# Kernel optimization log

Hardware: AMD Instinct MI355X
Metric: run time of the kernel (lower is better)

## Reference

```python
import jax, jax.numpy as jnp
import numpy as np

B, C, H, W = 4, 256, 96, 96
PARA, MOD, NH = 256, 256, 128
PI = 3.14159  # constant used in the torch source (not math.pi)


def setup_inputs():
    key = jax.random.key(0)
    ks = jax.random.split(key, 16)
    w = lambda k, shp: jax.random.normal(k, shp, jnp.float32) * 0.02
    z = lambda n: jnp.zeros((n,), jnp.float32)
    return {
        "feature_map": jax.random.normal(ks[0], (B, C, H, W), jnp.float32),
        "para_code": jax.random.normal(ks[1], (B, PARA), jnp.float32),
        "style_code": jax.random.normal(ks[2], (B, MOD), jnp.float32),
        "lin_common_w": w(ks[3], (PARA, PARA)), "lin_common_b": z(PARA),
        "lin_scale_w": w(ks[4], (PARA, C)), "lin_scale_b": z(C),
        "lin_rot_w": w(ks[5], (PARA, C)), "lin_rot_b": z(C),
        "lin_trans_w": w(ks[6], (PARA, 2 * C)), "lin_trans_b": z(2 * C),
        "a1_shared_w": w(ks[7], (MOD, NH)), "a1_shared_b": z(NH),
        "a1_gamma_w": w(ks[8], (NH, C)), "a1_gamma_b": z(C),
        "a1_beta_w": w(ks[9], (NH, C)), "a1_beta_b": z(C),
        "conv1_w": w(ks[10], (C, C, 3, 3)), "conv1_b": z(C),
        "a2_shared_w": w(ks[11], (MOD, NH)), "a2_shared_b": z(NH),
        "a2_gamma_w": w(ks[12], (NH, C)), "a2_gamma_b": z(C),
        "a2_beta_w": w(ks[13], (NH, C)), "a2_beta_b": z(C),
        "conv2_w": w(ks[14], (C, C, 3, 3)), "conv2_b": z(C),
    }


def _adaat(fm, pc, cw, cb, sw, sb, rw, rb, tw, tb):
    # fm: [B,C,H,W]; per-channel 2D affine warp, channels act as depth of a 3D grid_sample.
    Bn, Cn, Hn, Wn = fm.shape
    pc = jax.nn.relu(pc @ cw + cb)
    scale = jax.nn.sigmoid(pc @ sw + sb) * 2.0            # [B,C]
    angle = jnp.tanh(pc @ rw + rb) * PI                   # [B,C]
    trans = jnp.tanh(pc @ tw + tb).reshape(Bn, Cn, 2)     # [B,C,2]
    cos = jnp.cos(angle)[:, :, None, None]
    sin = jnp.sin(angle)[:, :, None, None]
    sc = scale[:, :, None, None]
    tx = trans[:, :, 0][:, :, None, None]
    ty = trans[:, :, 1][:, :, None, None]
    # align_corners=True style normalized source grid (as in make_coordinate_grid_3d)
    gx = (2.0 * jnp.arange(Wn) / (Wn - 1) - 1.0)[None, :]  # [1,W]
    gy = (2.0 * jnp.arange(Hn) / (Hn - 1) - 1.0)[:, None]  # [H,1]
    # rotation [[cos,-sin],[sin,cos]] @ [x,y], then scale + translate -> [B,C,H,W]
    xw = (cos * gx - sin * gy) * sc + tx
    yw = (sin * gx + cos * gy) * sc + ty
    gz = 2.0 * jnp.arange(Cn) / (Cn - 1) - 1.0             # [C]
    # unnormalize with align_corners=False (torch grid_sample default)
    ix = ((xw + 1.0) * Wn - 1.0) * 0.5
    iy = ((yw + 1.0) * Hn - 1.0) * 0.5
    iz = (((gz + 1.0) * Cn - 1.0) * 0.5)[None, :, None, None]  # [1,C,1,1]
    x0 = jnp.floor(ix); y0 = jnp.floor(iy); z0 = jnp.floor(iz)
    wx = ix - x0; wy = iy - y0; wz = iz - z0
    x0 = x0.astype(jnp.int32); y0 = y0.astype(jnp.int32); z0 = z0.astype(jnp.int32)
    bidx = jnp.arange(Bn)[:, None, None, None]

    def gather(zi, yi, xi):
        valid = (zi >= 0) & (zi < Cn) & (yi >= 0) & (yi < Hn) & (xi >= 0) & (xi < Wn)
        v = fm[bidx, jnp.clip(zi, 0, Cn - 1), jnp.clip(yi, 0, Hn - 1), jnp.clip(xi, 0, Wn - 1)]
        return jnp.where(valid, v, 0.0)

    out = jnp.zeros_like(fm)
    for dz, wzc in ((0, 1.0 - wz), (1, wz)):
        for dy, wyc in ((0, 1.0 - wy), (1, wy)):
            for dx, wxc in ((0, 1.0 - wx), (1, wx)):
                out = out + gather(z0 + dz, y0 + dy, x0 + dx) * (wzc * wyc * wxc)
    return out


def _adain_layer(x, style, shw, shb, gw, gb, bw, bb):
    m = x.mean(axis=(2, 3), keepdims=True)
    v = x.var(axis=(2, 3), keepdims=True)  # biased, as torch InstanceNorm2d
    xn = (x - m) / jnp.sqrt(v + 1e-5)
    a = jax.nn.relu(style @ shw + shb)
    gamma = (a @ gw + gb)[:, :, None, None]
    beta = (a @ bw + bb)[:, :, None, None]
    return xn * (1.0 + gamma) + beta


def _conv3(x, w, b):
    y = jax.lax.conv_general_dilated(x, w, (1, 1), ((1, 1), (1, 1)),
                                     dimension_numbers=("NCHW", "OIHW", "NCHW"))
    return y + b[None, :, None, None]


def _lrelu(x):
    return jnp.where(x >= 0, x, 0.2 * x)


def reference(feature_map, para_code, style_code,
              lin_common_w, lin_common_b, lin_scale_w, lin_scale_b,
              lin_rot_w, lin_rot_b, lin_trans_w, lin_trans_b,
              a1_shared_w, a1_shared_b, a1_gamma_w, a1_gamma_b, a1_beta_w, a1_beta_b,
              conv1_w, conv1_b,
              a2_shared_w, a2_shared_b, a2_gamma_w, a2_gamma_b, a2_beta_w, a2_beta_b,
              conv2_w, conv2_b):
    t = _adaat(feature_map, para_code, lin_common_w, lin_common_b,
               lin_scale_w, lin_scale_b, lin_rot_w, lin_rot_b, lin_trans_w, lin_trans_b)
    x = _adain_layer(t, style_code, a1_shared_w, a1_shared_b, a1_gamma_w, a1_gamma_b, a1_beta_w, a1_beta_b)
    x = _conv3(_lrelu(x), conv1_w, conv1_b)
    x = _adain_layer(x, style_code, a2_shared_w, a2_shared_b, a2_gamma_w, a2_gamma_b, a2_beta_w, a2_beta_b)
    x = _conv3(_lrelu(x), conv2_w, conv2_b)
    return x
```

## Files before the change

### kernel.cpp

```cpp
#include <hip/hip_runtime.h>
#include <hip/hip_bf16.h>
#include <cstddef>

#define BATCH 4
#define CH 256
#define HH 96
#define WW 96
#define HWN (HH*WW)
#define NTOT (BATCH*CH*HWN)
#define XT_H 98
#define XT_W 98
#define XT_PLANE (XT_H*XT_W*CH)

typedef __attribute__((ext_vector_type(16))) float f32x16;
typedef __attribute__((ext_vector_type(8))) __bf16 bfrag;
typedef __attribute__((ext_vector_type(8))) unsigned short u16x8;

static __device__ __forceinline__ unsigned short f2bf(float f) {
  unsigned int u = __float_as_uint(f);
  unsigned int r = (u + 0x7fffu + ((u >> 16) & 1u)) >> 16;
  return (unsigned short)r;
}

static __device__ __forceinline__ void gload16(const unsigned short* g,
                                               unsigned short* l) {
  __builtin_amdgcn_global_load_lds(
      (const __attribute__((address_space(1))) unsigned int*)g,
      (__attribute__((address_space(3))) unsigned int*)l, 16, 0, 0);
}

__global__ __launch_bounds__(256) void params_stage1_kernel(
    const float* __restrict__ para, const float* __restrict__ style,
    const float* __restrict__ cw,  const float* __restrict__ cb,
    const float* __restrict__ a1w, const float* __restrict__ a1b,
    const float* __restrict__ a2w, const float* __restrict__ a2b,
    float* __restrict__ pcbuf, float* __restrict__ a1buf, float* __restrict__ a2buf)
{
  __shared__ float s_in[256];
  __shared__ float red[256];
  int part = blockIdx.x, b = blockIdx.y, t = threadIdx.x;
  s_in[t] = (part < 4) ? para[b*256 + t] : style[b*256 + t];
  __syncthreads();
  if (part < 4) {
    int o = t & 63, ks = t >> 6, co0 = part * 64;
    const float* wcol = cw + co0 + o;
    float acc = 0.f;
    #pragma unroll 8
    for (int i = 0; i < 64; i++) {
      int k = ks * 64 + i;
      acc = fmaf(s_in[k], wcol[k * 256], acc);
    }
    red[t] = acc;
    __syncthreads();
    if (t < 64) {
      float s = red[t] + red[t + 64] + red[t + 128] + red[t + 192];
      pcbuf[b*256 + co0 + t] = fmaxf(s + cb[co0 + t], 0.f);
    }
  } else {
    const float* w  = (part == 4) ? a1w : a2w;
    const float* bb = (part == 4) ? a1b : a2b;
    float* outp = (part == 4) ? a1buf : a2buf;
    int o = t & 127, ks = t >> 7;
    const float* wcol = w + o;
    float acc = 0.f;
    #pragma unroll 8
    for (int i = 0; i < 128; i++) {
      int k = ks * 128 + i;
      acc = fmaf(s_in[k], wcol[k * 128], acc);
    }
    red[t] = acc;
    __syncthreads();
    if (t < 128) {
      float s = red[t] + red[t + 128];
      outp[b*128 + t] = fmaxf(s + bb[t], 0.f);
    }
  }
}

__global__ __launch_bounds__(256) void params_stage2_kernel(
    const float* __restrict__ pcbuf, const float* __restrict__ a1buf,
    const float* __restrict__ a2buf,
    const float* __restrict__ sw,  const float* __restrict__ sb,
    const float* __restrict__ rw,  const float* __restrict__ rb,
    const float* __restrict__ tw,  const float* __restrict__ tb,
    const float* __restrict__ g1w, const float* __restrict__ g1b,
    const float* __restrict__ b1w, const float* __restrict__ b1b,
    const float* __restrict__ g2w, const float* __restrict__ g2b,
    const float* __restrict__ b2w, const float* __restrict__ b2b,
    float* __restrict__ warp, float* __restrict__ gb1, float* __restrict__ gb2)
{
  __shared__ float s_pc[256], s_a1[128], s_a2[128];
  __shared__ float red[8][4][16];
  int co0 = blockIdx.x * 16, b = blockIdx.y, t = threadIdx.x;
  s_pc[t] = pcbuf[b*256 + t];
  if (t < 128) s_a1[t] = a1buf[b*128 + t];
  else         s_a2[t - 128] = a2buf[b*128 + (t - 128)];
  __syncthreads();

  int cl = t & 15, klane = t >> 4;
  int c = co0 + cl;
  const float2* tw2 = (const float2*)tw;
  float ds = 0.f, dr = 0.f, dtx = 0.f, dty = 0.f;
  float g1 = 0.f, be1 = 0.f, g2 = 0.f, be2 = 0.f;
  #pragma unroll 4
  for (int kk = 0; kk < 16; kk++) {
    int i = klane * 16 + kk;
    float p = s_pc[i];
    ds  = fmaf(p, sw[i*256 + c], ds);
    dr  = fmaf(p, rw[i*256 + c], dr);
    float2 tv = tw2[i*256 + c];
    dtx = fmaf(p, tv.x, dtx);
    dty = fmaf(p, tv.y, dty);
  }
  #pragma unroll 4
  for (int kk = 0; kk < 8; kk++) {
    int i = klane * 8 + kk;
    float a = s_a1[i];
    g1  = fmaf(a, g1w[i*256 + c], g1);
    be1 = fmaf(a, b1w[i*256 + c], be1);
    float a2v = s_a2[i];
    g2  = fmaf(a2v, g2w[i*256 + c], g2);
    be2 = fmaf(a2v, b2w[i*256 + c], be2);
  }
  ds  += __shfl_down(ds, 32, 64);  ds  += __shfl_down(ds, 16, 64);
  dr  += __shfl_down(dr, 32, 64);  dr  += __shfl_down(dr, 16, 64);
  dtx += __shfl_down(dtx, 32, 64); dtx += __shfl_down(dtx, 16, 64);
  dty += __shfl_down(dty, 32, 64); dty += __shfl_down(dty, 16, 64);
  g1  += __shfl_down(g1, 32, 64);  g1  += __shfl_down(g1, 16, 64);
  be1 += __shfl_down(be1, 32, 64); be1 += __shfl_down(be1, 16, 64);
  g2  += __shfl_down(g2, 32, 64);  g2  += __shfl_down(g2, 16, 64);
  be2 += __shfl_down(be2, 32, 64); be2 += __shfl_down(be2, 16, 64);
  int wv = t >> 6;
  if ((t & 63) < 16) {
    red[0][wv][cl] = ds;  red[1][wv][cl] = dr;
    red[2][wv][cl] = dtx; red[3][wv][cl] = dty;
    red[4][wv][cl] = g1;  red[5][wv][cl] = be1;
    red[6][wv][cl] = g2;  red[7][wv][cl] = be2;
  }
  __syncthreads();
  if (t < 16) {
    float v[8];
    #pragma unroll
    for (int o = 0; o < 8; o++)
      v[o] = red[o][0][t] + red[o][1][t] + red[o][2][t] + red[o][3][t];
    int cc = co0 + t;
    int bc = b*256 + cc;
    float scale = 2.f / (1.f + expf(-(v[0] + sb[cc])));
    float ang = tanhf(v[1] + rb[cc]) * 3.14159f;
    float sn, cs;
    sincosf(ang, &sn, &cs);
    warp[bc*4 + 0] = cs * scale;
    warp[bc*4 + 1] = sn * scale;
    warp[bc*4 + 2] = tanhf(v[2] + tb[2*cc]);
    warp[bc*4 + 3] = tanhf(v[3] + tb[2*cc + 1]);
    gb1[bc*2]     = v[4] + g1b[cc];
    gb1[bc*2 + 1] = v[5] + b1b[cc];
    gb2[bc*2]     = v[6] + g2b[cc];
    gb2[bc*2 + 1] = v[7] + b2b[cc];
  }
}

__global__ __launch_bounds__(256) void prep_weights_kernel(
    const float* __restrict__ w1, const float* __restrict__ w2,
    unsigned short* __restrict__ wf1, unsigned short* __restrict__ wf2)
{
  int co = blockIdx.x & 255;
  const float* src = (blockIdx.x < 256) ? w1 : w2;
  unsigned short* dst = (blockIdx.x < 256) ? wf1 : wf2;
  int ci = threadIdx.x;
  int coblk = co >> 6, m = (co >> 5) & 1;
  int l = (co & 31) | (((ci >> 3) & 1) << 5);
  int ks = ci >> 4, j = ci & 7;
  const float* p = src + ((size_t)co * 256 + ci) * 9;
  #pragma unroll
  for (int tap = 0; tap < 9; tap++) {
    size_t idx = (((size_t)((coblk * 16 + ks) * 9 + tap) * 2 + m) * 64 + l) * 8 + j;
    dst[idx] = f2bf(p[tap]);
  }
}

__global__ __launch_bounds__(256) void adaat_kernel(
    const float* __restrict__ fm, const float* __restrict__ warp,
    const float* __restrict__ gb1, float* __restrict__ tout,
    float* __restrict__ nrm1)
{
  __shared__ float s[96 * 100];
  int bc = blockIdx.x;
  int b = bc >> 8, c = bc & 255;
  float csc = warp[bc*4 + 0], ssc = warp[bc*4 + 1];
  float tx = warp[bc*4 + 2], ty = warp[bc*4 + 3];

  const float axw = csc * (96.f / 95.f);
  const float axh = -ssc * (96.f / 95.f);
  const float ax0 = 48.f * (tx - csc + ssc) + 47.5f;
  const float ayw = ssc * (96.f / 95.f);
  const float ayh = csc * (96.f / 95.f);
  const float ay0 = 48.f * (ty - ssc - csc) + 47.5f;

  float iz = 256.f * (float)c / 255.f - 0.5f;
  float z0f = floorf(iz);
  float wz = iz - z0f;
  int z0 = (int)z0f;
  const float* p0 = (z0 >= 0) ? fm + (size_t)(b*256 + z0) * HWN : nullptr;
  const float* p1 = (z0 + 1 < 256) ? fm + (size_t)(b*256 + z0 + 1) * HWN : nullptr;
  float w0 = 1.f - wz, w1 = wz;

  int t = threadIdx.x;
  const float4* q0 = (const float4*)p0;
  const float4* q1 = (const float4*)p1;
  for (int i = t; i < 2304; i += 256) {
    int row = i / 24, col = i - row * 24;
    float4 r = {0.f, 0.f, 0.f, 0.f};
    if (q0) {
      float4 v = q0[i];
      r.x = w0 * v.x; r.y = w0 * v.y; r.z = w0 * v.z; r.w = w0 * v.w;
    }
    if (q1) {
      float4 v = q1[i];
      r.x = fmaf(w1, v.x, r.x); r.y = fmaf(w1, v.y, r.y);
      r.z = fmaf(w1, v.z, r.z); r.w = fmaf(w1, v.w, r.w);
    }
    *(float4*)&s[row * 100 + col * 4] = r;
  }
  __syncthreads();

  int h = t / 96, w = t - (t / 96) * 96;
  float* dst = tout + (size_t)bc * HWN;
  float sum = 0.f, sumsq = 0.f;
  #pragma unroll
  for (int k = 0; k < 36; k++) {
    float ix = fmaf(axw, (float)w, fmaf(axh, (float)h, ax0));
    float iy = fmaf(ayw, (float)w, fmaf(ayh, (float)h, ay0));
    float x0f = floorf(ix), y0f = floorf(iy);
    float wx = ix - x0f, wy = iy - y0f;
    int x0 = (int)x0f, y0 = (int)y0f;
    int x0c = min(max(x0, 0), 95), x1c = min(max(x0 + 1, 0), 95);
    int y0c = min(max(y0, 0), 95), y1c = min(max(y0 + 1, 0), 95);
    bool vx0 = (unsigned)x0 < 96u, vx1 = (unsigned)(x0 + 1) < 96u;
    bool vy0 = (unsigned)y0 < 96u, vy1 = (unsigned)(y0 + 1) < 96u;
    float a00 = s[y0c * 100 + x0c], a01 = s[y0c * 100 + x1c];
    float a10 = s[y1c * 100 + x0c], a11 = s[y1c * 100 + x1c];
    float wxm = 1.f - wx, wym = 1.f - wy;
    float w00 = (vy0 && vx0) ? wym * wxm : 0.f;
    float w01 = (vy0 && vx1) ? wym * wx  : 0.f;
    float w10 = (vy1 && vx0) ? wy * wxm  : 0.f;
    float w11 = (vy1 && vx1) ? wy * wx   : 0.f;
    float v = w00 * a00;
    v = fmaf(w01, a01, v);
    v = fmaf(w10, a10, v);
    v = fmaf(w11, a11, v);
    dst[t + k * 256] = v;
    sum += v;
    sumsq = fmaf(v, v, sumsq);
    int wn = w + 64;
    int carry = (wn >= 96) ? 1 : 0;
    w = wn - (carry ? 96 : 0);
    h += 2 + carry;
  }

  for (int off = 32; off > 0; off >>= 1) {
    sum   += __shfl_down(sum, off, 64);
    sumsq += __shfl_down(sumsq, off, 64);
  }
  __shared__ float rs[4], rq[4];
  int lane = t & 63, wvi = t >> 6;
  if (lane == 0) { rs[wvi] = sum; rq[wvi] = sumsq; }
  __syncthreads();
  if (t == 0) {
    float S = rs[0] + rs[1] + rs[2] + rs[3];
    float Q = rq[0] + rq[1] + rq[2] + rq[3];
    float m = S * (1.f / 9216.f);
    float var = Q * (1.f / 9216.f) - m * m;
    float rstd = rsqrtf(var + 1e-5f);
    float sc = (1.f + gb1[bc*2]) * rstd;
    nrm1[bc*2] = sc;
    nrm1[bc*2 + 1] = gb1[bc*2 + 1] - m * sc;
  }
}

__global__ __launch_bounds__(256) void finalize_stats_kernel(
    const float* __restrict__ psum, const float* __restrict__ gb,
    float* __restrict__ nrm)
{
  int bc = blockIdx.x * 256 + threadIdx.x;
  int b = bc >> 8, co = bc & 255;
  float S = 0.f, Q = 0.f;
  for (int j = 0; j < 96; j++) {
    const float* p = psum + ((((size_t)b * 48 + (j >> 1)) * 2 + (j & 1)) * 256 + co) * 2;
    S += p[0];
    Q += p[1];
  }
  float m = S * (1.f / 9216.f);
  float var = Q * (1.f / 9216.f) - m * m;
  float rstd = rsqrtf(var + 1e-5f);
  float sc = (1.f + gb[bc*2]) * rstd;
  nrm[bc*2] = sc;
  nrm[bc*2 + 1] = gb[bc*2 + 1] - m * sc;
}

__global__ __launch_bounds__(256) void transpose_norm_kernel(
    const float* __restrict__ x, const float* __restrict__ nrm,
    unsigned short* __restrict__ xt)
{
  int hi = blockIdx.x;
  int b  = blockIdx.y;
  unsigned short* dst = xt + (size_t)b * XT_PLANE + (size_t)hi * (XT_W * CH);
  int t = threadIdx.x;
  int h = hi - 1;
  u16x8 zero = {0,0,0,0,0,0,0,0};
  if (h < 0 || h >= 96) {
    for (int c = t; c < XT_W * CH / 8; c += 256) ((u16x8*)dst)[c] = zero;
    return;
  }
  __shared__ unsigned short s[96 * 256];
  int ci = t;
  float sc = nrm[(b*256 + ci)*2], bi = nrm[(b*256 + ci)*2 + 1];
  const float* src = x + ((size_t)(b*256 + ci)) * HWN + h * 96;
  for (int wg = 0; wg < 24; wg++) {
    float4 v = *(const float4*)(src + wg * 4);
    float y0 = fmaf(v.x, sc, bi); y0 = (y0 >= 0.f) ? y0 : 0.2f * y0;
    float y1 = fmaf(v.y, sc, bi); y1 = (y1 >= 0.f) ? y1 : 0.2f * y1;
    float y2 = fmaf(v.z, sc, bi); y2 = (y2 >= 0.f) ? y2 : 0.2f * y2;
    float y3 = fmaf(v.w, sc, bi); y3 = (y3 >= 0.f) ? y3 : 0.2f * y3;
    s[(wg*4 + 0) * 256 + ci] = f2bf(y0);
    s[(wg*4 + 1) * 256 + ci] = f2bf(y1);
    s[(wg*4 + 2) * 256 + ci] = f2bf(y2);
    s[(wg*4 + 3) * 256 + ci] = f2bf(y3);
  }
  __syncthreads();
  for (int c = t; c < 98 * 32; c += 256) {
    int w = c >> 5, p = c & 31;
    u16x8 v = zero;
    if (w >= 1 && w <= 96) v = *(const u16x8*)&s[(w - 1) * 256 + p * 8];
    ((u16x8*)dst)[c] = v;
  }
}

__global__ __launch_bounds__(256, 3) void conv_mfma_kernel(
    const unsigned short* __restrict__ xt,
    const unsigned short* __restrict__ wf,
    const float* __restrict__ cb,
    float* __restrict__ out,
    float* __restrict__ psum)
{
  __shared__ __align__(16) unsigned short s_in[2][784 * 8];

  int hb = blockIdx.x, coblk = blockIdx.y, b = blockIdx.z;
  int co0 = coblk * 64, h0 = hb * 2;
  int t = threadIdx.x, lane = t & 63, wv = t >> 6;
  int rw = wv >> 1, mh = wv & 1;
  int l31 = lane & 31, lhi = lane >> 5;
  const unsigned short* xtb = xt + (size_t)b * XT_PLANE;

  int pre_g[4];
  #pragma unroll
  for (int i = 0; i < 4; i++) {
    int c = t + i * 256;
    if (c < 784) {
      int r = c / 196;
      int rem = c - r * 196;
      int half = rem / 98;
      int w = rem - half * 98;
      pre_g[i] = ((h0 + r) * 98 + w) * 256 + half * 8;
    }
  }

  f32x16 acc[3];
  #pragma unroll
  for (int n = 0; n < 3; n++)
    #pragma unroll
    for (int i = 0; i < 16; i++) acc[n][i] = 0.f;

  const unsigned short* wfb = wf + (size_t)(coblk * 16) * 9216 + mh * 512 + lane * 8;

  {
    #pragma unroll
    for (int i = 0; i < 3; i++)
      gload16(xtb + pre_g[i], &s_in[0][(i * 256 + wv * 64) * 8]);
    u16x8 tail;
    if (t < 16) tail = *(const u16x8*)(xtb + pre_g[3]);
    if (t < 16) *(u16x8*)(&s_in[0][(768 + t) * 8]) = tail;
  }
  bfrag wa[9];
  #pragma unroll
  for (int tap = 0; tap < 9; tap++) wa[tap] = *(const bfrag*)(wfb + tap * 1024);
  __syncthreads();

  int buf = 0;
  u16x8 tail;
  #pragma unroll 1
  for (int ks = 0; ks < 16; ks++) {
    if (ks < 15) {
      int cib = (ks + 1) * 16;
      unsigned short* nb = s_in[buf ^ 1];
      #pragma unroll
      for (int i = 0; i < 3; i++)
        gload16(xtb + pre_g[i] + cib, &nb[(i * 256 + wv * 64) * 8]);
      if (t < 16) tail = *(const u16x8*)(xtb + pre_g[3] + cib);
    }
    const unsigned short* sb = s_in[buf];
    int ksn = (ks < 15) ? (ks + 1) : 15;
    const unsigned short* wkn = wfb + (size_t)ksn * 9216;
    #pragma unroll
    for (int ky = 0; ky < 3; ky++) {
      const unsigned short* srow = sb + (((rw + ky) * 2 + lhi) * 98) * 8;
      bfrag bb[9];
      #pragma unroll
      for (int kx = 0; kx < 3; kx++)
        #pragma unroll
        for (int n = 0; n < 3; n++)
          bb[kx * 3 + n] = *(const bfrag*)(srow + (n * 32 + kx + l31) * 8);
      __builtin_amdgcn_s_setprio(1);
      #pragma unroll
      for (int kx = 0; kx < 3; kx++) {
        int tap = ky * 3 + kx;
        acc[0] = __builtin_amdgcn_mfma_f32_32x32x16_bf16(wa[tap], bb[kx*3+0], acc[0], 0, 0, 0);
        acc[1] = __builtin_amdgcn_mfma_f32_32x32x16_bf16(wa[tap], bb[kx*3+1], acc[1], 0, 0, 0);
        acc[2] = __builtin_amdgcn_mfma_f32_32x32x16_bf16(wa[tap], bb[kx*3+2], acc[2], 0, 0, 0);
        wa[tap] = *(const bfrag*)(wkn + tap * 1024);
      }
      __builtin_amdgcn_s_setprio(0);
    }
    if (ks < 15 && t < 16) *(u16x8*)(&s_in[buf ^ 1][(768 + t) * 8]) = tail;
    __syncthreads();
    buf ^= 1;
  }

  int h = h0 + rw;
  float bsum[16], bsq[16];
  #pragma unroll
  for (int r = 0; r < 16; r++) {
    int row = (r & 3) + 8 * (r >> 2) + 4 * lhi;
    int co = co0 + mh * 32 + row;
    float bv = cb[co];
    size_t base = ((size_t)(b * 256 + co) * 96 + h) * 96;
    float s = 0.f, q = 0.f;
    #pragma unroll
    for (int n = 0; n < 3; n++) {
      float y = acc[n][r] + bv;
      out[base + n * 32 + l31] = y;
      s += y;
      q = fmaf(y, y, q);
    }
    bsum[r] = s; bsq[r] = q;
  }
  if (psum) {
    #pragma unroll
    for (int r = 0; r < 16; r++) {
      float s = bsum[r], q = bsq[r];
      #pragma unroll
      for (int off = 16; off > 0; off >>= 1) {
        s += __shfl_xor(s, off, 64);
        q += __shfl_xor(q, off, 64);
      }
      bsum[r] = s; bsq[r] = q;
    }
    if (l31 == 0) {
      float* pp = psum + ((((size_t)b * 48 + hb) * 2 + rw) * 256) * 2;
      #pragma unroll
      for (int r = 0; r < 16; r++) {
        int row = (r & 3) + 8 * (r >> 2) + 4 * lhi;
        int co = co0 + mh * 32 + row;
        pp[co * 2]     = bsum[r];
        pp[co * 2 + 1] = bsq[r];
      }
    }
  }
}

extern "C" void kernel_launch(void* const* d_in, const int* in_sizes, int n_in,
                              void* d_out, int out_size, void* d_ws, size_t ws_size,
                              hipStream_t stream)
{
  const float* fm    = (const float*)d_in[0];
  const float* para  = (const float*)d_in[1];
  const float* style = (const float*)d_in[2];
  const float* cw  = (const float*)d_in[3];
  const float* cb  = (const float*)d_in[4];
  const float* sw  = (const float*)d_in[5];
  const float* sb  = (const float*)d_in[6];
  const float* rw  = (const float*)d_in[7];
  const float* rb  = (const float*)d_in[8];
  const float* tw  = (const float*)d_in[9];
  const float* tb  = (const float*)d_in[10];
  const float* a1w = (const float*)d_in[11];
  const float* a1b = (const float*)d_in[12];
  const float* g1w = (const float*)d_in[13];
  const float* g1b = (const float*)d_in[14];
  const float* b1w = (const float*)d_in[15];
  const float* b1b = (const float*)d_in[16];
  const float* c1w = (const float*)d_in[17];
  const float* c1b = (const float*)d_in[18];
  const float* a2w = (const float*)d_in[19];
  const float* a2b = (const float*)d_in[20];
  const float* g2w = (const float*)d_in[21];
  const float* g2b = (const float*)d_in[22];
  const float* b2w = (const float*)d_in[23];
  const float* b2b = (const float*)d_in[24];
  const float* c2w = (const float*)d_in[25];
  const float* c2b = (const float*)d_in[26];

  float* outf = (float*)d_out;

  unsigned short* xtbuf = (unsigned short*)d_ws;
  unsigned short* wf1   = xtbuf + (size_t)BATCH * XT_PLANE;
  unsigned short* wf2   = wf1 + 9 * 256 * 256;
  float* fws  = (float*)(wf2 + 9 * 256 * 256);
  float* warp = fws;
  float* gb1  = warp + 4 * 1024;
  float* gb2  = gb1 + 2 * 1024;
  float* nrm1 = gb2 + 2 * 1024;
  float* nrm2 = nrm1 + 2 * 1024;
  float* pcbuf = nrm2 + 2 * 1024;
  float* a1buf = pcbuf + 1024;
  float* a2buf = a1buf + 512;
  float* psum  = a2buf + 512;

  params_stage1_kernel<<<dim3(6, 4), 256, 0, stream>>>(para, style, cw, cb,
      a1w, a1b, a2w, a2b, pcbuf, a1buf, a2buf);
  params_stage2_kernel<<<dim3(16, 4), 256, 0, stream>>>(pcbuf, a1buf, a2buf,
      sw, sb, rw, rb, tw, tb, g1w, g1b, b1w, b1b, g2w, g2b, b2w, b2b,
      warp, gb1, gb2);
  prep_weights_kernel<<<512, 256, 0, stream>>>(c1w, c2w, wf1, wf2);
  adaat_kernel<<<1024, 256, 0, stream>>>(fm, warp, gb1, outf, nrm1);
  transpose_norm_kernel<<<dim3(98, 4), 256, 0, stream>>>(outf, nrm1, xtbuf);
  conv_mfma_kernel<<<dim3(48, 4, 4), 256, 0, stream>>>(xtbuf, wf1, c1b, outf, psum);
  finalize_stats_kernel<<<4, 256, 0, stream>>>(psum, gb2, nrm2);
  transpose_norm_kernel<<<dim3(98, 4), 256, 0, stream>>>(outf, nrm2, xtbuf);
  conv_mfma_kernel<<<dim3(48, 4, 4), 256, 0, stream>>>(xtbuf, wf2, c2b, outf, nullptr);
}
```

Measured before the change: 188.9 us.

## Give each conv wave both 32-channel output halves, halving block size

The conv kernel drops from 4 waves to 2 waves per block, and each wave now computes both 32-row output-channel halves (a 64x96 tile) instead of one. Each B fragment loaded from LDS is reused by two MFMAs, which halves LDS reads per MFMA and shrinks the block. The cost is double the accumulators and weight registers per thread (6 accumulators, 18 weight fragments), which pushes register pressure up. Launch bounds change to 128 threads with 2 blocks per SIMD hint, and each thread does twice as many staging loads.

```diff
diff --git a/kernel.cpp b/kernel.cpp
--- a/kernel.cpp
+++ b/kernel.cpp
@@ -336,7 +336,7 @@
   }
 }
 
-__global__ __launch_bounds__(256, 3) void conv_mfma_kernel(
+__global__ __launch_bounds__(128, 2) void conv_mfma_kernel(
     const unsigned short* __restrict__ xt,
     const unsigned short* __restrict__ wf,
     const float* __restrict__ cb,
@@ -348,62 +348,72 @@
   int hb = blockIdx.x, coblk = blockIdx.y, b = blockIdx.z;
   int co0 = coblk * 64, h0 = hb * 2;
   int t = threadIdx.x, lane = t & 63, wv = t >> 6;
-  int rw = wv >> 1, mh = wv & 1;
   int l31 = lane & 31, lhi = lane >> 5;
   const unsigned short* xtb = xt + (size_t)b * XT_PLANE;
 
-  int pre_g[4];
-  #pragma unroll
-  for (int i = 0; i < 4; i++) {
-    int c = t + i * 256;
-    if (c < 784) {
-      int r = c / 196;
-      int rem = c - r * 196;
-      int half = rem / 98;
-      int w = rem - half * 98;
-      pre_g[i] = ((h0 + r) * 98 + w) * 256 + half * 8;
-    }
-  }
-
-  f32x16 acc[3];
-  #pragma unroll
-  for (int n = 0; n < 3; n++)
+  int pre_g[6];
+  #pragma unroll
+  for (int i = 0; i < 6; i++) {
+    int c = t + i * 128;
+    int r = c / 196;
+    int rem = c - r * 196;
+    int half = rem / 98;
+    int w = rem - half * 98;
+    pre_g[i] = ((h0 + r) * 98 + w) * 256 + half * 8;
+  }
+  int tail_g = 0;
+  if (t < 16) {
+    int c = 768 + t;
+    int r = c / 196;
+    int rem = c - r * 196;
+    int half = rem / 98;
+    int w = rem - half * 98;
+    tail_g = ((h0 + r) * 98 + w) * 256 + half * 8;
+  }
+
+  f32x16 acc[2][3];
+  #pragma unroll
+  for (int m = 0; m < 2; m++)
     #pragma unroll
-    for (int i = 0; i < 16; i++) acc[n][i] = 0.f;
-
-  const unsigned short* wfb = wf + (size_t)(coblk * 16) * 9216 + mh * 512 + lane * 8;
-
-  {
-    #pragma unroll
-    for (int i = 0; i < 3; i++)
-      gload16(xtb + pre_g[i], &s_in[0][(i * 256 + wv * 64) * 8]);
-    u16x8 tail;
-    if (t < 16) tail = *(const u16x8*)(xtb + pre_g[3]);
-    if (t < 16) *(u16x8*)(&s_in[0][(768 + t) * 8]) = tail;
-  }
-  bfrag wa[9];
-  #pragma unroll
-  for (int tap = 0; tap < 9; tap++) wa[tap] = *(const bfrag*)(wfb + tap * 1024);
+    for (int n = 0; n < 3; n++)
+      #pragma unroll
+      for (int i = 0; i < 16; i++) acc[m][n][i] = 0.f;
+
+  const unsigned short* wfb = wf + (size_t)(coblk * 16) * 9216 + lane * 8;
+
+  #pragma unroll
+  for (int i = 0; i < 6; i++)
+    gload16(xtb + pre_g[i], &s_in[0][(i * 128 + wv * 64) * 8]);
+  u16x8 tl;
+  if (t < 16) {
+    tl = *(const u16x8*)(xtb + tail_g);
+    *(u16x8*)(&s_in[0][(768 + t) * 8]) = tl;
+  }
+  bfrag wa[9][2];
+  #pragma unroll
+  for (int tap = 0; tap < 9; tap++) {
+    wa[tap][0] = *(const bfrag*)(wfb + tap * 1024);
+    wa[tap][1] = *(const bfrag*)(wfb + tap * 1024 + 512);
+  }
   __syncthreads();
 
   int buf = 0;
-  u16x8 tail;
   #pragma unroll 1
   for (int ks = 0; ks < 16; ks++) {
     if (ks < 15) {
       int cib = (ks + 1) * 16;
       unsigned short* nb = s_in[buf ^ 1];
       #pragma unroll
-      for (int i = 0; i < 3; i++)
-        gload16(xtb + pre_g[i] + cib, &nb[(i * 256 + wv * 64) * 8]);
-      if (t < 16) tail = *(const u16x8*)(xtb + pre_g[3] + cib);
+      for (int i = 0; i < 6; i++)
+        gload16(xtb + pre_g[i] + cib, &nb[(i * 128 + wv * 64) * 8]);
+      if (t < 16) tl = *(const u16x8*)(xtb + tail_g + cib);
     }
     const unsigned short* sb = s_in[buf];
     int ksn = (ks < 15) ? (ks + 1) : 15;
     const unsigned short* wkn = wfb + (size_t)ksn * 9216;
     #pragma unroll
     for (int ky = 0; ky < 3; ky++) {
-      const unsigned short* srow = sb + (((rw + ky) * 2 + lhi) * 98) * 8;
+      const unsigned short* srow = sb + (((wv + ky) * 2 + lhi) * 98) * 8;
       bfrag bb[9];
       #pragma unroll
       for (int kx = 0; kx < 3; kx++)
@@ -414,56 +424,67 @@
       #pragma unroll
       for (int kx = 0; kx < 3; kx++) {
         int tap = ky * 3 + kx;
-        acc[0] = __builtin_amdgcn_mfma_f32_32x32x16_bf16(wa[tap], bb[kx*3+0], acc[0], 0, 0, 0);
-        acc[1] = __builtin_amdgcn_mfma_f32_32x32x16_bf16(wa[tap], bb[kx*3+1], acc[1], 0, 0, 0);
-        acc[2] = __builtin_amdgcn_mfma_f32_32x32x16_bf16(wa[tap], bb[kx*3+2], acc[2], 0, 0, 0);
-        wa[tap] = *(const bfrag*)(wkn + tap * 1024);
+        acc[0][0] = __builtin_amdgcn_mfma_f32_32x32x16_bf16(wa[tap][0], bb[kx*3+0], acc[0][0], 0, 0, 0);
+        acc[1][0] = __builtin_amdgcn_mfma_f32_32x32x16_bf16(wa[tap][1], bb[kx*3+0], acc[1][0], 0, 0, 0);
+        acc[0][1] = __builtin_amdgcn_mfma_f32_32x32x16_bf16(wa[tap][0], bb[kx*3+1], acc[0][1], 0, 0, 0);
+        acc[1][1] = __builtin_amdgcn_mfma_f32_32x32x16_bf16(wa[tap][1], bb[kx*3+1], acc[1][1], 0, 0, 0);
+        acc[0][2] = __builtin_amdgcn_mfma_f32_32x32x16_bf16(wa[tap][0], bb[kx*3+2], acc[0][2], 0, 0, 0);
+        acc[1][2] = __builtin_amdgcn_mfma_f32_32x32x16_bf16(wa[tap][1], bb[kx*3+2], acc[1][2], 0, 0, 0);
+        wa[tap][0] = *(const bfrag*)(wkn + tap * 1024);
+        wa[tap][1] = *(const bfrag*)(wkn + tap * 1024 + 512);
       }
       __builtin_amdgcn_s_setprio(0);
     }
-    if (ks < 15 && t < 16) *(u16x8*)(&s_in[buf ^ 1][(768 + t) * 8]) = tail;
+    if (ks < 15 && t < 16) *(u16x8*)(&s_in[buf ^ 1][(768 + t) * 8]) = tl;
     __syncthreads();
     buf ^= 1;
   }
 
-  int h = h0 + rw;
-  float bsum[16], bsq[16];
-  #pragma unroll
-  for (int r = 0; r < 16; r++) {
-    int row = (r & 3) + 8 * (r >> 2) + 4 * lhi;
-    int co = co0 + mh * 32 + row;
-    float bv = cb[co];
-    size_t base = ((size_t)(b * 256 + co) * 96 + h) * 96;
-    float s = 0.f, q = 0.f;
+  int h = h0 + wv;
+  float bsum[2][16], bsq[2][16];
+  #pragma unroll
+  for (int m = 0; m < 2; m++) {
     #pragma unroll
-    for (int n = 0; n < 3; n++) {
-      float y = acc[n][r] + bv;
-      out[base + n * 32 + l31] = y;
-      s += y;
-      q = fmaf(y, y, q);
-    }
-    bsum[r] = s; bsq[r] = q;
+    for (int r = 0; r < 16; r++) {
+      int row = (r & 3) + 8 * (r >> 2) + 4 * lhi;
+      int co = co0 + m * 32 + row;
+      float bv = cb[co];
+      size_t base = ((size_t)(b * 256 + co) * 96 + h) * 96;
+      float s = 0.f, q = 0.f;
+      #pragma unroll
+      for (int n = 0; n < 3; n++) {
+        float y = acc[m][n][r] + bv;
+        out[base + n * 32 + l31] = y;
+        s += y;
+        q = fmaf(y, y, q);
+      }
+      bsum[m][r] = s; bsq[m][r] = q;
+    }
   }
   if (psum) {
     #pragma unroll
-    for (int r = 0; r < 16; r++) {
-      float s = bsum[r], q = bsq[r];
-      #pragma unroll
-      for (int off = 16; off > 0; off >>= 1) {
-        s += __shfl_xor(s, off, 64);
-        q += __shfl_xor(q, off, 64);
+    for (int m = 0; m < 2; m++)
+      #pragma unroll
+      for (int r = 0; r < 16; r++) {
+        float s = bsum[m][r], q = bsq[m][r];
+        #pragma unroll
+        for (int off = 16; off > 0; off >>= 1) {
+          s += __shfl_xor(s, off, 64);
+          q += __shfl_xor(q, off, 64);
+        }
+        bsum[m][r] = s; bsq[m][r] = q;
       }
-      bsum[r] = s; bsq[r] = q;
-    }
     if (l31 == 0) {
-      float* pp = psum + ((((size_t)b * 48 + hb) * 2 + rw) * 256) * 2;
-      #pragma unroll
-      for (int r = 0; r < 16; r++) {
-        int row = (r & 3) + 8 * (r >> 2) + 4 * lhi;
-        int co = co0 + mh * 32 + row;
-        pp[co * 2]     = bsum[r];
-        pp[co * 2 + 1] = bsq[r];
-      }
+      float* pp = psum + ((((size_t)b * 48 + hb) * 2 + wv) * 256) * 2;
+      #pragma unroll
+      for (int m = 0; m < 2; m++)
+        #pragma unroll
+        for (int r = 0; r < 16; r++) {
+          int row = (r & 3) + 8 * (r >> 2) + 4 * lhi;
+          int co = co0 + m * 32 + row;
+          pp[co * 2]     = bsum[m][r];
+          pp[co * 2 + 1] = bsq[m][r];
+        }
     }
   }
 }
@@ -524,8 +545,8 @@
   prep_weights_kernel<<<512, 256, 0, stream>>>(c1w, c2w, wf1, wf2);
   adaat_kernel<<<1024, 256, 0, stream>>>(fm, warp, gb1, outf, nrm1);
   transpose_norm_kernel<<<dim3(98, 4), 256, 0, stream>>>(outf, nrm1, xtbuf);
-  conv_mfma_kernel<<<dim3(48, 4, 4), 256, 0, stream>>>(xtbuf, wf1, c1b, outf, psum);
+  conv_mfma_kernel<<<dim3(48, 4, 4), 128, 0, stream>>>(xtbuf, wf1, c1b, outf, psum);
   finalize_stats_kernel<<<4, 256, 0, stream>>>(psum, gb2, nrm2);
   transpose_norm_kernel<<<dim3(98, 4), 256, 0, stream>>>(outf, nrm2, xtbuf);
-  conv_mfma_kernel<<<dim3(48, 4, 4), 256, 0, stream>>>(xtbuf, wf2, c2b, outf, nullptr);
-}
+  conv_mfma_kernel<<<dim3(48, 4, 4), 128, 0, stream>>>(xtbuf, wf2, c2b, outf, nullptr);
+}
```

Result: no change. 188.1 us (-0.4%).

## Emit conv1 output as bf16 NHWC directly and normalize in place

Applied to the files above, without the earlier changes.

The first conv epilogue now stages its bf16 results in shared memory and writes them straight into a second padded NHWC buffer, instead of writing fp32 NCHW output. A new lightweight norm2 kernel applies the AdaIN scale/bias and leaky ReLU in place on that buffer, replacing the transpose_norm pass. This removes an fp32 write and re-read plus a transpose between the two convs. In exchange it adds a second workspace plane, an extra sync and shared-memory staging in the epilogue, and rounds conv1 outputs to bf16 before normalization, while the statistics are still computed in fp32.

```diff
diff --git a/kernel.cpp b/kernel.cpp
--- a/kernel.cpp
+++ b/kernel.cpp
@@ -20,6 +20,9 @@
   unsigned int u = __float_as_uint(f);
   unsigned int r = (u + 0x7fffu + ((u >> 16) & 1u)) >> 16;
   return (unsigned short)r;
+}
+static __device__ __forceinline__ float bf2f(unsigned short s) {
+  return __uint_as_float(((unsigned int)s) << 16);
 }
 
 static __device__ __forceinline__ void gload16(const unsigned short* g,
@@ -336,14 +339,50 @@
   }
 }
 
+__global__ __launch_bounds__(256) void norm2_kernel(
+    unsigned short* __restrict__ xt, const float* __restrict__ nrm)
+{
+  int hi = blockIdx.x, b = blockIdx.y;
+  unsigned short* row = xt + (size_t)b * XT_PLANE + (size_t)hi * (XT_W * CH);
+  int t = threadIdx.x;
+  u16x8 zero = {0,0,0,0,0,0,0,0};
+  if (hi == 0 || hi == 97) {
+    for (int c = t; c < XT_W * CH / 8; c += 256) ((u16x8*)row)[c] = zero;
+    return;
+  }
+  int p = t & 31;
+  float sc[8], bi[8];
+  #pragma unroll
+  for (int j = 0; j < 8; j++) {
+    int co = p * 8 + j;
+    sc[j] = nrm[(b*256 + co)*2];
+    bi[j] = nrm[(b*256 + co)*2 + 1];
+  }
+  for (int wi = t >> 5; wi < 98; wi += 8) {
+    int c = wi * 32 + p;
+    if (wi == 0 || wi == 97) { ((u16x8*)row)[c] = zero; continue; }
+    u16x8 v = ((u16x8*)row)[c];
+    u16x8 o;
+    #pragma unroll
+    for (int j = 0; j < 8; j++) {
+      float x = bf2f(v[j]);
+      float y = fmaf(x, sc[j], bi[j]);
+      y = (y >= 0.f) ? y : 0.2f * y;
+      o[j] = f2bf(y);
+    }
+    ((u16x8*)row)[c] = o;
+  }
+}
+
 __global__ __launch_bounds__(256, 3) void conv_mfma_kernel(
     const unsigned short* __restrict__ xt,
     const unsigned short* __restrict__ wf,
     const float* __restrict__ cb,
     float* __restrict__ out,
+    unsigned short* __restrict__ xt2,
     float* __restrict__ psum)
 {
-  __shared__ __align__(16) unsigned short s_in[2][784 * 8];
+  __shared__ __align__(16) unsigned short s_in[2][6528];
 
   int hb = blockIdx.x, coblk = blockIdx.y, b = blockIdx.z;
   int co0 = coblk * 64, h0 = hb * 2;
@@ -377,9 +416,9 @@
     #pragma unroll
     for (int i = 0; i < 3; i++)
       gload16(xtb + pre_g[i], &s_in[0][(i * 256 + wv * 64) * 8]);
-    u16x8 tail;
-    if (t < 16) tail = *(const u16x8*)(xtb + pre_g[3]);
-    if (t < 16) *(u16x8*)(&s_in[0][(768 + t) * 8]) = tail;
+    u16x8 tail0;
+    if (t < 16) tail0 = *(const u16x8*)(xtb + pre_g[3]);
+    if (t < 16) *(u16x8*)(&s_in[0][(768 + t) * 8]) = tail0;
   }
   bfrag wa[9];
   #pragma unroll
@@ -427,24 +466,25 @@
   }
 
   int h = h0 + rw;
-  float bsum[16], bsq[16];
-  #pragma unroll
-  for (int r = 0; r < 16; r++) {
-    int row = (r & 3) + 8 * (r >> 2) + 4 * lhi;
-    int co = co0 + mh * 32 + row;
-    float bv = cb[co];
-    size_t base = ((size_t)(b * 256 + co) * 96 + h) * 96;
-    float s = 0.f, q = 0.f;
-    #pragma unroll
-    for (int n = 0; n < 3; n++) {
-      float y = acc[n][r] + bv;
-      out[base + n * 32 + l31] = y;
-      s += y;
-      q = fmaf(y, y, q);
-    }
-    bsum[r] = s; bsq[r] = q;
-  }
   if (psum) {
+    unsigned short* tb = (unsigned short*)s_in;
+    float bsum[16], bsq[16];
+    #pragma unroll
+    for (int r = 0; r < 16; r++) {
+      int row = (r & 3) + 8 * (r >> 2) + 4 * lhi;
+      int col = mh * 32 + row;
+      float bv = cb[co0 + col];
+      float s = 0.f, q = 0.f;
+      #pragma unroll
+      for (int n = 0; n < 3; n++) {
+        float y = acc[n][r] + bv;
+        int px = n * 32 + l31;
+        tb[(rw * 96 + px) * 68 + col] = f2bf(y);
+        s += y;
+        q = fmaf(y, y, q);
+      }
+      bsum[r] = s; bsq[r] = q;
+    }
     #pragma unroll
     for (int r = 0; r < 16; r++) {
       float s = bsum[r], q = bsq[r];
@@ -463,6 +503,33 @@
         int co = co0 + mh * 32 + row;
         pp[co * 2]     = bsum[r];
         pp[co * 2 + 1] = bsq[r];
+      }
+    }
+    __syncthreads();
+    unsigned short* dstb = xt2 + (size_t)b * XT_PLANE;
+    #pragma unroll
+    for (int i = 0; i < 6; i++) {
+      int c = t + i * 256;
+      int row2 = c / 768;
+      int rem = c - row2 * 768;
+      int wi = rem >> 3, p8 = rem & 7;
+      const unsigned short* lsrc = &tb[(row2 * 96 + wi) * 68 + p8 * 8];
+      uint2 lo = *(const uint2*)lsrc;
+      uint2 hi2 = *(const uint2*)(lsrc + 4);
+      size_t ga = ((size_t)(h0 + 1 + row2) * 98 + (wi + 1)) * 256 + co0 + p8 * 8;
+      uint4 vv; vv.x = lo.x; vv.y = lo.y; vv.z = hi2.x; vv.w = hi2.y;
+      *(uint4*)&dstb[ga] = vv;
+    }
+  } else {
+    #pragma unroll
+    for (int r = 0; r < 16; r++) {
+      int row = (r & 3) + 8 * (r >> 2) + 4 * lhi;
+      int co = co0 + mh * 32 + row;
+      float bv = cb[co];
+      size_t base = ((size_t)(b * 256 + co) * 96 + h) * 96;
+      #pragma unroll
+      for (int n = 0; n < 3; n++) {
+        out[base + n * 32 + l31] = acc[n][r] + bv;
       }
     }
   }
@@ -502,9 +569,10 @@
 
   float* outf = (float*)d_out;
 
-  unsigned short* xtbuf = (unsigned short*)d_ws;
-  unsigned short* wf1   = xtbuf + (size_t)BATCH * XT_PLANE;
-  unsigned short* wf2   = wf1 + 9 * 256 * 256;
+  unsigned short* xtbuf  = (unsigned short*)d_ws;
+  unsigned short* xt2buf = xtbuf + (size_t)BATCH * XT_PLANE;
+  unsigned short* wf1    = xt2buf + (size_t)BATCH * XT_PLANE;
+  unsigned short* wf2    = wf1 + 9 * 256 * 256;
   float* fws  = (float*)(wf2 + 9 * 256 * 256);
   float* warp = fws;
   float* gb1  = warp + 4 * 1024;
@@ -524,8 +592,10 @@
   prep_weights_kernel<<<512, 256, 0, stream>>>(c1w, c2w, wf1, wf2);
   adaat_kernel<<<1024, 256, 0, stream>>>(fm, warp, gb1, outf, nrm1);
   transpose_norm_kernel<<<dim3(98, 4), 256, 0, stream>>>(outf, nrm1, xtbuf);
-  conv_mfma_kernel<<<dim3(48, 4, 4), 256, 0, stream>>>(xtbuf, wf1, c1b, outf, psum);
+  conv_mfma_kernel<<<dim3(48, 4, 4), 256, 0, stream>>>(xtbuf, wf1, c1b,
+      outf, xt2buf, psum);
   finalize_stats_kernel<<<4, 256, 0, stream>>>(psum, gb2, nrm2);
-  transpose_norm_kernel<<<dim3(98, 4), 256, 0, stream>>>(outf, nrm2, xtbuf);
-  conv_mfma_kernel<<<dim3(48, 4, 4), 256, 0, stream>>>(xtbuf, wf2, c2b, outf, nullptr);
-}
+  norm2_kernel<<<dim3(98, 4), 256, 0, stream>>>(xt2buf, nrm2);
+  conv_mfma_kernel<<<dim3(48, 4, 4), 256, 0, stream>>>(xt2buf, wf2, c2b,
+      outf, nullptr, nullptr);
+}
```

After: 185.1 us. 2.0% less time.
